# Performance work log

Measured on AMD Instinct MI355X. Metric: run time of the kernel, lower is better.

## Reference

```python
import jax, jax.numpy as jnp
import numpy as np

B, T, H, NH, DH, R = 2, 2048, 1024, 16, 64, 256
ALPHA = 0.6


def setup_inputs() -> dict:
    key = jax.random.key(0)
    ks = jax.random.split(key, 28)
    f32 = jnp.float32

    def nrm(k, shape, s=0.02):
        return jax.random.normal(k, shape, dtype=f32) * s

    inp = {}
    inp['x'] = jax.random.normal(ks[0], (B, T, H), dtype=f32)
    # additive causal mask [1,1,T,T]: 0 on/below diagonal, -1e9 above
    causal = jnp.tril(jnp.ones((T, T), dtype=bool))
    inp['attention_mask'] = jnp.where(causal, 0.0, -1e9).astype(f32)[None, None]
    # low-rank SVD factors for q,k,v,o: Vh [H,R], S [R] (positive), U [H,R], b [H]
    i = 1
    for name in ('q', 'k', 'v', 'o'):
        inp['Vh_' + name] = nrm(ks[i], (H, R)); i += 1
        inp['S_' + name] = jax.random.uniform(ks[i], (R,), dtype=f32, minval=0.5, maxval=1.5); i += 1
        inp['U_' + name] = nrm(ks[i], (H, R)); i += 1
        inp['b_' + name] = jnp.zeros((H,), dtype=f32); i += 1
    # full-rank weights of the original (fallback) attention: y = x @ W + b (Conv1D style)
    for name in ('q', 'k', 'v', 'o'):
        inp['W_' + name] = nrm(ks[i], (H, H)); i += 1
        inp['bf_' + name] = jnp.zeros((H,), dtype=f32); i += 1
    return inp


def _split_heads(t):
    # [B,T,H] -> [B,nH,T,dH]
    Bs, Ts, _ = t.shape
    return t.reshape(Bs, Ts, NH, DH).transpose(0, 2, 1, 3)


def _attention(Q, K, V, mask):
    q, k, v = _split_heads(Q), _split_heads(K), _split_heads(V)
    scores = jnp.einsum('bhtd,bhsd->bhts', q, k) / (DH ** 0.5)
    scores = scores + mask
    w = jax.nn.softmax(scores, axis=-1)
    ctx = jnp.einsum('bhts,bhsd->bhtd', w, v)
    Bs = ctx.shape[0]
    return ctx.transpose(0, 2, 1, 3).reshape(Bs, -1, NH * DH)


def _lowrank(x, Vh, S, U, b):
    # ((x @ Vh) * S) @ U.T + b
    return ((x @ Vh) * S) @ U.T + b


def reference(x, attention_mask,
              Vh_q, S_q, U_q, b_q, Vh_k, S_k, U_k, b_k,
              Vh_v, S_v, U_v, b_v, Vh_o, S_o, U_o, b_o,
              W_q, bf_q, W_k, bf_k, W_v, bf_v, W_o, bf_o):
    # --- low-rank SVD path ---
    Q = _lowrank(x, Vh_q, S_q, U_q, b_q)
    K = _lowrank(x, Vh_k, S_k, U_k, b_k)
    V = _lowrank(x, Vh_v, S_v, U_v, b_v)
    ctx = _attention(Q, K, V, attention_mask)
    out = _lowrank(ctx, Vh_o, S_o, U_o, b_o)
    # --- fallback: original full-rank attention ---
    Qf = x @ W_q + bf_q
    Kf = x @ W_k + bf_k
    Vf = x @ W_v + bf_v
    ctxf = _attention(Qf, Kf, Vf, attention_mask)
    fallback_out = ctxf @ W_o + bf_o
    return ALPHA * out + (1.0 - ALPHA) * fallback_out
```

## Files before the change

kernel.cpp:

```cpp
#include <hip/hip_runtime.h>
#include <hip/hip_bf16.h>

typedef __bf16 bf16_t;
typedef __bf16 bf16x8 __attribute__((ext_vector_type(8)));
typedef float f32x4 __attribute__((ext_vector_type(4)));
typedef _Float16 f16_t;
typedef _Float16 f16x4 __attribute__((ext_vector_type(4)));

extern "C" __device__ float __ocml_native_exp2_f32(float);

#define DEVI static __device__ __forceinline__

static constexpr int TN   = 2048;
static constexpr int Hn   = 1024;
static constexpr int Rn   = 256;
static constexpr int MTOK = 4096;
static constexpr int NCAT = 6144;

static constexpr float QSCALE = 0.125f;
static constexpr float LOG2E  = 1.44269504088896340736f;
static constexpr float SOFT_OFF2 = 0.426950408889634f;

template <typename T>
DEVI void gload16(const T* g, T* l) {
    __builtin_amdgcn_global_load_lds(
        (const __attribute__((address_space(1))) void*)g,
        (__attribute__((address_space(3))) void*)l, 16, 0, 0);
}

DEVI float loadf(const void* base, int idx, bool bfm) {
    if (bfm) {
        unsigned int u = ((const unsigned short*)base)[idx];
        u <<= 16;
        return __builtin_bit_cast(float, u);
    }
    return ((const float*)base)[idx];
}
DEVI bool detect_bf16(const void* mask) {
    return fabsf(((const float*)mask)[0]) > 1.0f;
}

struct PrepArgs {
    const void *x, *mask;
    const void *Vh[4], *S[4], *U[4];
    const void *bb[4], *bfb[4];
    bf16_t *Xb, *Abuf, *Bbuf;
    float *biascat, *biaso;
};

__global__ void k_prep(PrepArgs a) {
    const bool bfm = detect_bf16(a.mask);
    const int bid = blockIdx.x;
    if (bid < 4096) {
        int i = (bid * 256 + threadIdx.x) * 4;
#pragma unroll
        for (int j = 0; j < 4; ++j) a.Xb[i + j] = (bf16_t)loadf(a.x, i + j, bfm);
    } else if (bid < 8192) {
        int idx = (bid - 4096) * 256 + threadIdx.x;
        int proj = idx >> 18;
        int e = idx & 262143;
        int r = e & 255;
        float s = loadf(a.S[proj], r, bfm);
        if (proj == 0) s *= QSCALE * LOG2E;
        if (proj == 3) s *= 0.6f;
        a.Abuf[idx] = (bf16_t)(loadf(a.U[proj], e, bfm) * s);
        a.Bbuf[idx] = (bf16_t)loadf(a.Vh[proj], e, bfm);
    } else {
        int i = (bid - 8192) * 256 + threadIdx.x;
        if (i < 1024)      a.biascat[i] = QSCALE * LOG2E * loadf(a.bb[0], i, bfm);
        else if (i < 2048) a.biascat[i] = loadf(a.bb[1], i - 1024, bfm);
        else if (i < 3072) a.biascat[i] = loadf(a.bb[2], i - 2048, bfm);
        else if (i < 4096) a.biascat[i] = QSCALE * LOG2E * loadf(a.bfb[0], i - 3072, bfm);
        else if (i < 5120) a.biascat[i] = loadf(a.bfb[1], i - 4096, bfm);
        else if (i < 6144) a.biascat[i] = loadf(a.bfb[2], i - 5120, bfm);
        else {
            int j = i - 6144;
            a.biaso[j] = 0.6f * loadf(a.bb[3], j, bfm) + 0.4f * loadf(a.bfb[3], j, bfm);
        }
    }
}

struct TransP { const void* W[4]; bf16_t* dst[4]; int ldd[4]; float scale[4]; const void* mask; };

__global__ void k_transpose4(TransP tp) {
    const bool bfm = detect_bf16(tp.mask);
    const int z = blockIdx.z;
    const void* W = tp.W[z];
    bf16_t* dst = tp.dst[z];
    const int ldd = tp.ldd[z];
    const float scale = tp.scale[z];
    __shared__ float t[32][33];
    int bx = blockIdx.x * 32, by = blockIdx.y * 32;
    int tx = threadIdx.x, ty = threadIdx.y;
#pragma unroll
    for (int k = 0; k < 32; k += 8)
        t[ty + k][tx] = loadf(W, (by + ty + k) * Hn + bx + tx, bfm);
    __syncthreads();
#pragma unroll
    for (int k = 0; k < 32; k += 8)
        dst[(size_t)(bx + ty + k) * ldd + by + tx] = (bf16_t)(scale * t[tx][ty + k]);
}

template <int MI>
DEVI void gemm_core64(const bf16_t* __restrict__ A, int lda,
                      const bf16_t* __restrict__ B, int ldb, int K,
                      bf16_t* A0, bf16_t* A1, bf16_t* B0, bf16_t* B1,
                      int bm, int bn, f32x4 (&acc)[MI][4]) {
    constexpr int MT = MI * 32;
    const int tid  = threadIdx.x;
    const int lane = tid & 63;
    const int w    = tid >> 6;
    const int wr   = (w >> 1) * (MI * 16);
    const int wc   = (w & 1) * 64;
    const int fr   = lane & 15;
    const int quad = lane >> 4;

#pragma unroll
    for (int i = 0; i < MI; ++i)
#pragma unroll
        for (int j = 0; j < 4; ++j) acc[i][j] = {0.f, 0.f, 0.f, 0.f};

    for (int kb = 0; kb < K; kb += 64) {
        __syncthreads();
        for (int u = tid; u < MT * 4; u += 256) {
            const bf16_t* as = &A[(size_t)(bm + (u >> 2)) * lda + kb + (u & 3) * 8];
            gload16(as,      &A0[u * 8]);
            gload16(as + 32, &A1[u * 8]);
        }
#pragma unroll
        for (int t = 0; t < 2; ++t) {
            int u = t * 256 + tid;
            const bf16_t* bs = &B[(size_t)(bn + (u >> 2)) * ldb + kb + (u & 3) * 8];
            gload16(bs,      &B0[u * 8]);
            gload16(bs + 32, &B1[u * 8]);
        }
        __syncthreads();

#pragma unroll
        for (int kk = 0; kk < 2; ++kk) {
            const bf16_t* Ap = kk ? A1 : A0;
            const bf16_t* Bp = kk ? B1 : B0;
            bf16x8 af[MI], bfv[4];
#pragma unroll
            for (int i = 0; i < MI; ++i)
                af[i] = *(const bf16x8*)&Ap[(wr + i * 16 + fr) * 32 + quad * 8];
#pragma unroll
            for (int j = 0; j < 4; ++j)
                bfv[j] = *(const bf16x8*)&Bp[(wc + j * 16 + fr) * 32 + quad * 8];
#pragma unroll
            for (int i = 0; i < MI; ++i)
#pragma unroll
                for (int j = 0; j < 4; ++j)
                    acc[i][j] = __builtin_amdgcn_mfma_f32_16x16x32_bf16(af[i], bfv[j], acc[i][j], 0, 0, 0);
        }
    }
}

template <int MI, bool OUT_DUAL, bool WRITE_VT>
__global__ __launch_bounds__(256)
void k_gemm(const bf16_t* __restrict__ A, int lda,
            const bf16_t* __restrict__ B, int ldb,
            void* __restrict__ C, int ldc, int K,
            const float* __restrict__ bias, const void* __restrict__ mask,
            f16_t* __restrict__ Vt_g) {
    constexpr int MT = MI * 32;
    struct GB { bf16_t A0[MT * 32]; bf16_t A1[MT * 32]; bf16_t B0[4096]; bf16_t B1[4096]; };
    union SM { GB g; f16_t Ls[WRITE_VT ? 128 * 136 : 8]; };
    __shared__ __align__(16) SM sm;

    const int tid  = threadIdx.x;
    const int lane = tid & 63;
    const int w    = tid >> 6;
    const int wr   = (w >> 1) * (MI * 16);
    const int wc   = (w & 1) * 64;
    const int bm   = blockIdx.x * MT;
    const int bn   = blockIdx.y * 128;
    const int fr   = lane & 15;
    const int quad = lane >> 4;

    f32x4 acc[MI][4];
    gemm_core64<MI>(A, lda, B, ldb, K, sm.g.A0, sm.g.A1, sm.g.B0, sm.g.B1, bm, bn, acc);

    if constexpr (WRITE_VT) {
        const bool isV = (bn >= 2048 && bn < 3072) || (bn >= 5120);
        if (isV) {
            const int pth = (bn >= 5120) ? 1 : 0;
            const int colrel = bn - (pth ? 5120 : 2048);
            const int bb = bm >> 11;
            const int R0 = (pth * 32 + bb * 16 + (colrel >> 6)) * 64;
            const int tloc = bm & 2047;
            __syncthreads();
#pragma unroll
            for (int i = 0; i < MI; ++i) {
                const int t0 = wr + i * 16 + quad * 4;
#pragma unroll
                for (int j = 0; j < 4; ++j) {
                    const int c = wc + j * 16 + fr;
                    const float bv = bias[bn + c];
#pragma unroll
                    for (int r = 0; r < 4; ++r)
                        sm.Ls[c * 136 + t0 + r] = (f16_t)(acc[i][j][r] + bv);
                }
            }
            __syncthreads();
            const int c = tid >> 1, seg = tid & 1;
            f16_t* dst = &Vt_g[(size_t)(R0 + c) * TN + tloc + seg * 64];
            const f16_t* src = &sm.Ls[c * 136 + seg * 64];
#pragma unroll
            for (int e = 0; e < 8; ++e)
                *(uint4*)&dst[e * 8] = *(const uint4*)&src[e * 8];
            return;
        }
    }

    bool bfm = false;
    if constexpr (OUT_DUAL) bfm = detect_bf16(mask);
#pragma unroll
    for (int i = 0; i < MI; ++i) {
        const int row0 = bm + wr + i * 16 + quad * 4;
#pragma unroll
        for (int j = 0; j < 4; ++j) {
            const int col = bn + wc + j * 16 + fr;
            const float bv = bias ? bias[col] : 0.f;
#pragma unroll
            for (int r = 0; r < 4; ++r) {
                float v = acc[i][j][r] + bv;
                size_t ci = (size_t)(row0 + r) * ldc + col;
                if constexpr (OUT_DUAL) {
                    if (bfm) ((unsigned short*)C)[ci] = __builtin_bit_cast(unsigned short, (bf16_t)v);
                    else     ((float*)C)[ci] = v;
                } else {
                    ((bf16_t*)C)[ci] = (bf16_t)v;
                }
            }
        }
    }
}

__global__ __launch_bounds__(512, 2)
void k_gemm8(const bf16_t* __restrict__ A, int lda,
             const bf16_t* __restrict__ B, int ldb,
             bf16_t* __restrict__ C, int ldc, int K,
             const float* __restrict__ bias, f16_t* __restrict__ Vt_g) {
    struct Pipe { bf16_t At[4][256 * 32]; bf16_t Bt[4][128 * 32]; };
    union SM8 { Pipe p; f16_t Ls[128 * 264]; };
    __shared__ __align__(16) SM8 sm;

    const int tid  = threadIdx.x;
    const int lane = tid & 63;
    const int wid  = tid >> 6;
    const int wr   = (wid >> 1) * 64;
    const int wc   = (wid & 1) * 64;
    const int fr   = lane & 15;
    const int quad = lane >> 4;

    const int bid = blockIdx.x;
    const int bm  = (bid & 15) * 256;
    const int bn  = (bid >> 4) * 128;

    const int csrc = ((tid & 3) ^ ((tid >> 3) & 3)) * 8;
    const int ksw  = (quad ^ ((fr >> 1) & 3)) * 8;
    const int raB  = (wr + fr) * 32 + ksw;
    const int rbB  = (wc + fr) * 32 + ksw;
    const int r0   = tid >> 2;

    auto stage = [&](int sidx) {
        const int slot = sidx & 3;
        const int kb = sidx * 32;
        gload16(&A[(size_t)(bm + r0) * lda + kb + csrc],       &sm.p.At[slot][tid * 8]);
        gload16(&A[(size_t)(bm + 128 + r0) * lda + kb + csrc], &sm.p.At[slot][(512 + tid) * 8]);
        gload16(&B[(size_t)(bn + r0) * ldb + kb + csrc],       &sm.p.Bt[slot][tid * 8]);
    };

    f32x4 acc[4][4];
#pragma unroll
    for (int i = 0; i < 4; ++i)
#pragma unroll
        for (int j = 0; j < 4; ++j) acc[i][j] = {0.f, 0.f, 0.f, 0.f};

    const int NS = K >> 5;
    stage(0); stage(1); stage(2);

    for (int s = 0; s < NS; ++s) {
        if (s + 3 < NS) {
            stage(s + 3);
            asm volatile("s_waitcnt vmcnt(9)" ::: "memory");
        } else if (s + 3 == NS) {
            asm volatile("s_waitcnt vmcnt(6)" ::: "memory");
        } else if (s + 2 == NS) {
            asm volatile("s_waitcnt vmcnt(3)" ::: "memory");
        } else {
            asm volatile("s_waitcnt vmcnt(0)" ::: "memory");
        }
        __builtin_amdgcn_s_barrier();
        __builtin_amdgcn_sched_barrier(0);

        const int slot = s & 3;
        bf16x8 af[4], bv[4];
#pragma unroll
        for (int i = 0; i < 4; ++i)
            af[i] = *(const bf16x8*)&sm.p.At[slot][raB + i * 512];
#pragma unroll
        for (int j = 0; j < 4; ++j)
            bv[j] = *(const bf16x8*)&sm.p.Bt[slot][rbB + j * 512];

        __builtin_amdgcn_s_setprio(1);
#pragma unroll
        for (int i = 0; i < 4; ++i)
#pragma unroll
            for (int j = 0; j < 4; ++j)
                acc[i][j] = __builtin_amdgcn_mfma_f32_16x16x32_bf16(af[i], bv[j], acc[i][j], 0, 0, 0);
        __builtin_amdgcn_s_setprio(0);

        __builtin_amdgcn_s_barrier();
        __builtin_amdgcn_sched_barrier(0);
    }

    const bool isV = (bn >= 2048 && bn < 3072) || (bn >= 5120);
    if (isV) {
        const int pth = (bn >= 5120) ? 1 : 0;
        const int pbase = pth ? 5120 : 2048;
        const int bb = bm >> 11;
        const int vrow0 = (pth * 32 + bb * 16) * 64 + (bn - pbase);
        const int tloc = bm & 2047;
        __syncthreads();
#pragma unroll
        for (int j = 0; j < 4; ++j) {
            const int c = wc + j * 16 + fr;
            const float bv = bias[bn + c];
#pragma unroll
            for (int i = 0; i < 4; ++i) {
                const int t0 = wr + i * 16 + quad * 4;
                f16x4 pk;
#pragma unroll
                for (int r = 0; r < 4; ++r) pk[r] = (f16_t)(acc[i][j][r] + bv);
                *(f16x4*)&sm.Ls[c * 264 + t0] = pk;
            }
        }
        __syncthreads();
        const int c = tid >> 2, seg = tid & 3;
        f16_t* dst = &Vt_g[(size_t)(vrow0 + c) * TN + tloc + seg * 64];
        const f16_t* src = &sm.Ls[c * 264 + seg * 64];
#pragma unroll
        for (int e = 0; e < 8; ++e)
            *(uint4*)&dst[e * 8] = *(const uint4*)&src[e * 8];
        return;
    }

#pragma unroll
    for (int i = 0; i < 4; ++i) {
        const int row0 = bm + wr + i * 16 + quad * 4;
#pragma unroll
        for (int j = 0; j < 4; ++j) {
            const int col = bn + wc + j * 16 + fr;
            const float bv = bias[col];
#pragma unroll
            for (int r = 0; r < 4; ++r)
                C[(size_t)(row0 + r) * ldc + col] = (bf16_t)(acc[i][j][r] + bv);
        }
    }
}

__global__ __launch_bounds__(256)
void k_gemm_small4(const bf16_t* __restrict__ Abuf, const bf16_t* __restrict__ Bbuf,
                   bf16_t* __restrict__ Wcat, bf16_t* __restrict__ WoT) {
    __shared__ __align__(16) bf16_t A0[64 * 32], A1[64 * 32], B0[4096], B1[4096];
    const int z = blockIdx.z;
    const bf16_t* A = Abuf + (size_t)z * Hn * Rn;
    const bf16_t* B = Bbuf + (size_t)z * Hn * Rn;
    bf16_t* C = (z < 3) ? (Wcat + (size_t)z * Hn * Hn) : WoT;
    const int ldc = (z < 3) ? Hn : 2048;

    const int bm = blockIdx.x * 64, bn = blockIdx.y * 128;
    f32x4 acc[2][4];
    gemm_core64<2>(A, Rn, B, Rn, Rn, A0, A1, B0, B1, bm, bn, acc);

    const int lane = threadIdx.x & 63;
    const int w    = threadIdx.x >> 6;
    const int wr   = (w >> 1) * 32;
    const int wc   = (w & 1) * 64;
    const int fr   = lane & 15;
    const int quad = lane >> 4;
#pragma unroll
    for (int i = 0; i < 2; ++i)
#pragma unroll
        for (int j = 0; j < 4; ++j)
#pragma unroll
            for (int r = 0; r < 4; ++r)
                C[(size_t)(bm + wr + i * 16 + quad * 4 + r) * ldc + bn + wc + j * 16 + fr]
                    = (bf16_t)acc[i][j][r];
}

__global__ __launch_bounds__(256, 4)
void k_flash6(const bf16_t* __restrict__ Y, const f16_t* __restrict__ Vt_g,
              bf16_t* __restrict__ Ctx) {
    const int id   = blockIdx.x;
    const int inst = id & 63;
    const int slot = (id >> 6) & 3;
    const int rnd  = id >> 8;
    const int qt2  = (rnd == 0) ? 15 - slot
                   : (rnd == 1) ? 11 - slot
                   : (rnd == 2) ? 4 + slot
                                : slot;
    const int p = inst >> 5, b = (inst >> 4) & 1, h = inst & 15;

    const int tid  = threadIdx.x;
    const int lane = tid & 63;
    const int w    = tid >> 6;
    const int fr   = lane & 15;
    const int quad = lane >> 4;

    const int rowbase = b * TN;
    const int qbase   = qt2 * 128;
    const int qcol = p * 3072 + h * 64;
    const int kcol = qcol + 1024;
    const int ccol = p * 1024 + h * 64;

    __shared__ __align__(16) bf16_t Kb[2][2][64 * 32];
    __shared__ __align__(16) f16_t  Vb[2][64 * 64];

    const int r64 = tid >> 2;
    const int c8s = (((tid & 3) ^ ((tid >> 4) & 3)) * 8);
    const int ksw = (quad ^ ((fr >> 2) & 3)) * 8;

    size_t vsrc[2];
#pragma unroll
    for (int t = 0; t < 2; ++t) {
        int pp = w * 128 + t * 64 + lane;
        int d  = pp >> 3;
        vsrc[t] = (size_t)(inst * 64 + d) * TN + ((((pp & 7) - d) & 7) * 8);
    }

    f16x4 ones;
#pragma unroll
    for (int j = 0; j < 4; ++j) ones[j] = (f16_t)1.0f;

    const f32x4 off4 = {-SOFT_OFF2, -SOFT_OFF2, -SOFT_OFF2, -SOFT_OFF2};

    bf16x8 qf[2][2];
#pragma unroll
    for (int s = 0; s < 2; ++s) {
        const size_t qrow = (size_t)(rowbase + qbase + s * 64 + w * 16 + fr) * NCAT + qcol;
        qf[s][0] = *(const bf16x8*)&Y[qrow + quad * 8];
        qf[s][1] = *(const bf16x8*)&Y[qrow + 32 + quad * 8];
    }

    f32x4 o[2][4], lacc[2];
#pragma unroll
    for (int s = 0; s < 2; ++s) {
        lacc[s] = {0.f, 0.f, 0.f, 0.f};
#pragma unroll
        for (int db = 0; db < 4; ++db) o[s][db] = {0.f, 0.f, 0.f, 0.f};
    }

    const int t0 = (quad >> 1) + (fr & 7);
    const int h4 = (quad & 1) * 4;
    int voff[4];
#pragma unroll
    for (int nb = 0; nb < 4; ++nb) voff[nb] = ((nb * 2 + t0) & 7) * 8;

    const int kl = quad * 4;
    const int ql = w * 16 + fr;

    const int kmax = 2 * qt2 + 1;

    auto stage = [&](int kt, int bsel) {
        const bf16_t* ksrc = &Y[(size_t)(rowbase + kt * 64 + r64) * NCAT + kcol + c8s];
        gload16(ksrc,      &Kb[bsel][0][tid * 8]);
        gload16(ksrc + 32, &Kb[bsel][1][tid * 8]);
#pragma unroll
        for (int t = 0; t < 2; ++t)
            gload16(&Vt_g[vsrc[t] + kt * 64], &Vb[bsel][(w * 128 + t * 64 + lane) * 8]);
    };

    stage(0, 0);

    for (int kt = 0; kt <= kmax; ++kt) {
        const int cur = kt & 1;
        __syncthreads();
        if (kt < kmax) stage(kt + 1, cur ^ 1);

        const bool a0 = (kt < kmax);

        f16x4 pf[2][4];
#pragma unroll
        for (int nb = 0; nb < 4; ++nb) {
            const int ka = (nb * 16 + fr) * 32 + ksw;
            bf16x8 kf0 = *(const bf16x8*)&Kb[cur][0][ka];
            bf16x8 kf1 = *(const bf16x8*)&Kb[cur][1][ka];
#pragma unroll
            for (int s = 0; s < 2; ++s) {
                if (s == 0 && !a0) continue;
                f32x4 t4 = __builtin_amdgcn_mfma_f32_16x16x32_bf16(kf0, qf[s][0], off4, 0, 0, 0);
                t4 = __builtin_amdgcn_mfma_f32_16x16x32_bf16(kf1, qf[s][1], t4, 0, 0, 0);
                if (kt == 2 * qt2 + s) {
#pragma unroll
                    for (int r = 0; r < 4; ++r)
                        if (nb * 16 + kl + r > ql) t4[r] = -1e30f;
                }
                auto lo = __builtin_amdgcn_cvt_pkrtz(__ocml_native_exp2_f32(t4[0]),
                                                     __ocml_native_exp2_f32(t4[1]));
                auto hi = __builtin_amdgcn_cvt_pkrtz(__ocml_native_exp2_f32(t4[2]),
                                                     __ocml_native_exp2_f32(t4[3]));
                pf[s][nb] = __builtin_bit_cast(f16x4, __builtin_shufflevector(lo, hi, 0, 1, 2, 3));
            }
        }

#pragma unroll
        for (int s = 0; s < 2; ++s) {
            if (s == 0 && !a0) continue;
#pragma unroll
            for (int nb = 0; nb < 4; ++nb)
                lacc[s] = __builtin_amdgcn_mfma_f32_16x16x16f16(pf[s][nb], ones, lacc[s], 0, 0, 0);
        }

#pragma unroll
        for (int db = 0; db < 4; ++db) {
            const int vbase = (db * 16 + fr) * 64 + h4;
            f16x4 vf[4];
#pragma unroll
            for (int nb = 0; nb < 4; ++nb)
                vf[nb] = *(const f16x4*)&Vb[cur][vbase + voff[nb]];
#pragma unroll
            for (int nb = 0; nb < 4; ++nb) {
                o[1][db] = __builtin_amdgcn_mfma_f32_16x16x16f16(pf[1][nb], vf[nb], o[1][db], 0, 0, 0);
                if (a0)
                    o[0][db] = __builtin_amdgcn_mfma_f32_16x16x16f16(pf[0][nb], vf[nb], o[0][db], 0, 0, 0);
            }
        }
    }

#pragma unroll
    for (int s = 0; s < 2; ++s)
#pragma unroll
        for (int r = 0; r < 4; ++r) {
            const float inv = 1.0f / lacc[s][r];
            const size_t trow = (size_t)(rowbase + qbase + s * 64 + w * 16 + quad * 4 + r);
#pragma unroll
            for (int db = 0; db < 4; ++db)
                Ctx[trow * 2048 + ccol + db * 16 + fr] = (bf16_t)(o[s][db][r] * inv);
        }
}

extern "C" void kernel_launch(void* const* d_in, const int* in_sizes, int n_in,
                              void* d_out, int out_size, void* d_ws, size_t ws_size,
                              hipStream_t stream) {
    const void* x    = d_in[0];
    const void* mask = d_in[1];
    const void* Vh[4] = { d_in[2],  d_in[6],  d_in[10], d_in[14] };
    const void* Sp[4] = { d_in[3],  d_in[7],  d_in[11], d_in[15] };
    const void* Up[4] = { d_in[4],  d_in[8],  d_in[12], d_in[16] };
    const void* bb[4] = { d_in[5],  d_in[9],  d_in[13], d_in[17] };
    const void* Wp[4] = { d_in[18], d_in[20], d_in[22], d_in[24] };
    const void* bf[4] = { d_in[19], d_in[21], d_in[23], d_in[25] };

    char* ws = (char*)d_ws;
    size_t off = 0;
    auto alloc = [&](size_t bytes) -> void* {
        void* p = ws + off;
        off = (off + bytes + 255) & ~(size_t)255;
        return p;
    };
    bf16_t* Xb      = (bf16_t*)alloc((size_t)MTOK * Hn * 2);
    bf16_t* Wcat    = (bf16_t*)alloc((size_t)NCAT * Hn * 2);
    bf16_t* Yb      = (bf16_t*)alloc((size_t)MTOK * NCAT * 2);
    bf16_t* Ctx     = (bf16_t*)alloc((size_t)MTOK * 2048 * 2);
    bf16_t* WoT     = (bf16_t*)alloc((size_t)Hn * 2048 * 2);
    f16_t*  Vt_g    = (f16_t*)alloc((size_t)64 * 64 * TN * 2);
    bf16_t* Abuf    = (bf16_t*)alloc((size_t)4 * Hn * Rn * 2);
    bf16_t* Bbuf    = (bf16_t*)alloc((size_t)4 * Hn * Rn * 2);
    float*  biascat = (float*)alloc(NCAT * 4);
    float*  biaso   = (float*)alloc(Hn * 4);

    PrepArgs pa;
    pa.x = x; pa.mask = mask;
    for (int i = 0; i < 4; ++i) {
        pa.Vh[i] = Vh[i]; pa.S[i] = Sp[i]; pa.U[i] = Up[i];
        pa.bb[i] = bb[i]; pa.bfb[i] = bf[i];
    }
    pa.Xb = Xb; pa.Abuf = Abuf; pa.Bbuf = Bbuf; pa.biascat = biascat; pa.biaso = biaso;
    k_prep<<<8220, 256, 0, stream>>>(pa);

    TransP tp;
    for (int i = 0; i < 3; ++i) {
        tp.W[i] = Wp[i]; tp.dst[i] = Wcat + (size_t)(3 * Hn + i * Hn) * Hn;
        tp.ldd[i] = Hn; tp.scale[i] = (i == 0) ? QSCALE * LOG2E : 1.0f;
    }
    tp.W[3] = Wp[3]; tp.dst[3] = WoT + 1024; tp.ldd[3] = 2048; tp.scale[3] = 0.4f;
    tp.mask = mask;
    k_transpose4<<<dim3(32, 32, 4), dim3(32, 8), 0, stream>>>(tp);

    k_gemm_small4<<<dim3(16, 8, 4), 256, 0, stream>>>(Abuf, Bbuf, Wcat, WoT);

    k_gemm8<<<768, 512, 0, stream>>>(
        Xb, Hn, Wcat, Hn, Yb, NCAT, Hn, biascat, Vt_g);

    k_flash6<<<1024, 256, 0, stream>>>(Yb, Vt_g, Ctx);

    k_gemm<2, true, false><<<dim3(64, 8), 256, 0, stream>>>(
        Ctx, 2048, WoT, 2048, d_out, Hn, 2048, biaso, mask, nullptr);
}
```

Measured before the change: 304.7 us.

## Restructure QKV GEMM to 4 waves with 128x64 warp tiles and register prefetch

```diff
diff --git a/kernel.cpp b/kernel.cpp
--- a/kernel.cpp
+++ b/kernel.cpp
@@ -237,19 +237,19 @@
     }
 }
 
-__global__ __launch_bounds__(512, 2)
+__global__ __launch_bounds__(256, 2)
 void k_gemm8(const bf16_t* __restrict__ A, int lda,
              const bf16_t* __restrict__ B, int ldb,
              bf16_t* __restrict__ C, int ldc, int K,
              const float* __restrict__ bias, f16_t* __restrict__ Vt_g) {
-    struct Pipe { bf16_t At[4][256 * 32]; bf16_t Bt[4][128 * 32]; };
+    struct Pipe { bf16_t As[3][256 * 32]; bf16_t Bs[3][128 * 32]; };
     union SM8 { Pipe p; f16_t Ls[128 * 264]; };
     __shared__ __align__(16) SM8 sm;
 
     const int tid  = threadIdx.x;
     const int lane = tid & 63;
     const int wid  = tid >> 6;
-    const int wr   = (wid >> 1) * 64;
+    const int wr   = (wid >> 1) * 128;
     const int wc   = (wid & 1) * 64;
     const int fr   = lane & 15;
     const int quad = lane >> 4;
@@ -259,59 +259,73 @@
     const int bn  = (bid >> 4) * 128;
 
     const int csrc = ((tid & 3) ^ ((tid >> 3) & 3)) * 8;
-    const int ksw  = (quad ^ ((fr >> 1) & 3)) * 8;
-    const int raB  = (wr + fr) * 32 + ksw;
-    const int rbB  = (wc + fr) * 32 + ksw;
+    const int ksw8 = (quad ^ ((fr >> 1) & 3)) * 8;
+    const int raB  = (wr + fr) * 32 + ksw8;
+    const int rbB  = (wc + fr) * 32 + ksw8;
     const int r0   = tid >> 2;
 
     auto stage = [&](int sidx) {
-        const int slot = sidx & 3;
+        const int slot = sidx % 3;
         const int kb = sidx * 32;
-        gload16(&A[(size_t)(bm + r0) * lda + kb + csrc],       &sm.p.At[slot][tid * 8]);
-        gload16(&A[(size_t)(bm + 128 + r0) * lda + kb + csrc], &sm.p.At[slot][(512 + tid) * 8]);
-        gload16(&B[(size_t)(bn + r0) * ldb + kb + csrc],       &sm.p.Bt[slot][tid * 8]);
+        const bf16_t* a0 = &A[(size_t)(bm + r0) * lda + kb + csrc];
+        gload16(a0,                       &sm.p.As[slot][tid * 8]);
+        gload16(a0 + (size_t)64  * lda,   &sm.p.As[slot][(256 + tid) * 8]);
+        gload16(a0 + (size_t)128 * lda,   &sm.p.As[slot][(512 + tid) * 8]);
+        gload16(a0 + (size_t)192 * lda,   &sm.p.As[slot][(768 + tid) * 8]);
+        const bf16_t* b0 = &B[(size_t)(bn + r0) * ldb + kb + csrc];
+        gload16(b0,                       &sm.p.Bs[slot][tid * 8]);
+        gload16(b0 + (size_t)64 * ldb,    &sm.p.Bs[slot][(256 + tid) * 8]);
     };
 
-    f32x4 acc[4][4];
-#pragma unroll
-    for (int i = 0; i < 4; ++i)
+    f32x4 acc[8][4];
+#pragma unroll
+    for (int i = 0; i < 8; ++i)
 #pragma unroll
         for (int j = 0; j < 4; ++j) acc[i][j] = {0.f, 0.f, 0.f, 0.f};
 
     const int NS = K >> 5;
-    stage(0); stage(1); stage(2);
+    stage(0); stage(1);
+    asm volatile("s_waitcnt vmcnt(6)" ::: "memory");
+    __builtin_amdgcn_s_barrier();
+    __builtin_amdgcn_sched_barrier(0);
+
+    bf16x8 af[8], bv[4];
+    {
+        const bf16_t* Ap = sm.p.As[0];
+        const bf16_t* Bp = sm.p.Bs[0];
+#pragma unroll
+        for (int i = 0; i < 8; ++i) af[i] = *(const bf16x8*)&Ap[raB + i * 512];
+#pragma unroll
+        for (int j = 0; j < 4; ++j) bv[j] = *(const bf16x8*)&Bp[rbB + j * 512];
+    }
 
     for (int s = 0; s < NS; ++s) {
-        if (s + 3 < NS) {
-            stage(s + 3);
-            asm volatile("s_waitcnt vmcnt(9)" ::: "memory");
-        } else if (s + 3 == NS) {
+        if (s + 2 < NS) {
+            stage(s + 2);
             asm volatile("s_waitcnt vmcnt(6)" ::: "memory");
         } else if (s + 2 == NS) {
-            asm volatile("s_waitcnt vmcnt(3)" ::: "memory");
-        } else {
             asm volatile("s_waitcnt vmcnt(0)" ::: "memory");
         }
         __builtin_amdgcn_s_barrier();
         __builtin_amdgcn_sched_barrier(0);
 
-        const int slot = s & 3;
-        bf16x8 af[4], bv[4];
-#pragma unroll
-        for (int i = 0; i < 4; ++i)
-            af[i] = *(const bf16x8*)&sm.p.At[slot][raB + i * 512];
-#pragma unroll
-        for (int j = 0; j < 4; ++j)
-            bv[j] = *(const bf16x8*)&sm.p.Bt[slot][rbB + j * 512];
-
         __builtin_amdgcn_s_setprio(1);
 #pragma unroll
-        for (int i = 0; i < 4; ++i)
+        for (int i = 0; i < 8; ++i)
 #pragma unroll
             for (int j = 0; j < 4; ++j)
                 acc[i][j] = __builtin_amdgcn_mfma_f32_16x16x32_bf16(af[i], bv[j], acc[i][j], 0, 0, 0);
         __builtin_amdgcn_s_setprio(0);
 
+        if (s + 1 < NS) {
+            const int slot = (s + 1) % 3;
+            const bf16_t* Ap = sm.p.As[slot];
+            const bf16_t* Bp = sm.p.Bs[slot];
+#pragma unroll
+            for (int i = 0; i < 8; ++i) af[i] = *(const bf16x8*)&Ap[raB + i * 512];
+#pragma unroll
+            for (int j = 0; j < 4; ++j) bv[j] = *(const bf16x8*)&Bp[rbB + j * 512];
+        }
         __builtin_amdgcn_s_barrier();
         __builtin_amdgcn_sched_barrier(0);
     }
@@ -323,40 +337,39 @@
         const int bb = bm >> 11;
         const int vrow0 = (pth * 32 + bb * 16) * 64 + (bn - pbase);
         const int tloc = bm & 2047;
-        __syncthreads();
 #pragma unroll
         for (int j = 0; j < 4; ++j) {
             const int c = wc + j * 16 + fr;
-            const float bv = bias[bn + c];
-#pragma unroll
-            for (int i = 0; i < 4; ++i) {
+            const float bvv = bias[bn + c];
+#pragma unroll
+            for (int i = 0; i < 8; ++i) {
                 const int t0 = wr + i * 16 + quad * 4;
                 f16x4 pk;
 #pragma unroll
-                for (int r = 0; r < 4; ++r) pk[r] = (f16_t)(acc[i][j][r] + bv);
+                for (int r = 0; r < 4; ++r) pk[r] = (f16_t)(acc[i][j][r] + bvv);
                 *(f16x4*)&sm.Ls[c * 264 + t0] = pk;
             }
         }
         __syncthreads();
-        const int c = tid >> 2, seg = tid & 3;
-        f16_t* dst = &Vt_g[(size_t)(vrow0 + c) * TN + tloc + seg * 64];
-        const f16_t* src = &sm.Ls[c * 264 + seg * 64];
-#pragma unroll
-        for (int e = 0; e < 8; ++e)
+        const int c = tid >> 1, seg = tid & 1;
+        f16_t* dst = &Vt_g[(size_t)(vrow0 + c) * TN + tloc + seg * 128];
+        const f16_t* src = &sm.Ls[c * 264 + seg * 128];
+#pragma unroll
+        for (int e = 0; e < 16; ++e)
             *(uint4*)&dst[e * 8] = *(const uint4*)&src[e * 8];
         return;
     }
 
 #pragma unroll
-    for (int i = 0; i < 4; ++i) {
+    for (int i = 0; i < 8; ++i) {
         const int row0 = bm + wr + i * 16 + quad * 4;
 #pragma unroll
         for (int j = 0; j < 4; ++j) {
             const int col = bn + wc + j * 16 + fr;
-            const float bv = bias[col];
+            const float bvv = bias[col];
 #pragma unroll
             for (int r = 0; r < 4; ++r)
-                C[(size_t)(row0 + r) * ldc + col] = (bf16_t)(acc[i][j][r] + bv);
+                C[(size_t)(row0 + r) * ldc + col] = (bf16_t)(acc[i][j][r] + bvv);
         }
     }
 }
@@ -592,7 +605,7 @@
 
     k_gemm_small4<<<dim3(16, 8, 4), 256, 0, stream>>>(Abuf, Bbuf, Wcat, WoT);
 
-    k_gemm8<<<768, 512, 0, stream>>>(
+    k_gemm8<<<768, 256, 0, stream>>>(
         Xb, Hn, Wcat, Hn, Yb, NCAT, Hn, biascat, Vt_g);
 
     k_flash6<<<1024, 256, 0, stream>>>(Yb, Vt_g, Ctx);
```

Result: no change. 299.6 us (-1.7%).
